# Optimization experiments

Measured on AMD Instinct MI355X. Metric: run time of the kernel, lower is better.

The kernel has to match this reference:

```python
import jax, jax.numpy as jnp
import numpy as np


def _apply_1q(state, U, wire):
    # state: (B,) + (2,)*n big-endian (wire 0 = axis 1, Pennylane convention)
    # U: (2,2) shared or (B,2,2) per-sample
    s = jnp.moveaxis(state, wire + 1, 1)
    eq = 'bij,bj...->bi...' if U.ndim == 3 else 'ij,bj...->bi...'
    s = jnp.einsum(eq, U, s)
    return jnp.moveaxis(s, 1, wire + 1)


def _rx(theta):  # theta: (B,) -> (B,2,2)
    c = jnp.cos(theta / 2).astype(jnp.complex64)
    s = (-1j * jnp.sin(theta / 2)).astype(jnp.complex64)
    return jnp.stack([jnp.stack([c, s], -1), jnp.stack([s, c], -1)], -2)


def _ry(theta):  # theta: (B,) -> (B,2,2)
    c = jnp.cos(theta / 2).astype(jnp.complex64)
    s = jnp.sin(theta / 2).astype(jnp.complex64)
    return jnp.stack([jnp.stack([c, -s], -1), jnp.stack([s, c], -1)], -2)


def _rot(phi, theta, omega):  # Pennylane Rot = RZ(omega) RY(theta) RZ(phi)
    c = jnp.cos(theta / 2)
    s = jnp.sin(theta / 2)
    r0 = jnp.stack([jnp.exp(-1j * (phi + omega) / 2) * c,
                    -jnp.exp(1j * (phi - omega) / 2) * s])
    r1 = jnp.stack([jnp.exp(-1j * (phi - omega) / 2) * s,
                    jnp.exp(1j * (phi + omega) / 2) * c])
    return jnp.stack([r0, r1]).astype(jnp.complex64)


def _cnot_adj(state, ctrl):
    # CNOT(control=ctrl, target=ctrl+1): flip target axis on control=1 slice
    a0 = jax.lax.index_in_dim(state, 0, ctrl + 1, keepdims=True)
    a1 = jax.lax.index_in_dim(state, 1, ctrl + 1, keepdims=True)
    return jnp.concatenate([a0, jnp.flip(a1, axis=ctrl + 2)], axis=ctrl + 1)


def _forward(state_batch, weights, head_w, head_b):
    L, n, _ = weights.shape
    B = state_batch.shape[0]
    psi = jnp.zeros((B, 2 ** n), jnp.complex64).at[:, 0].set(1.0)
    psi = psi.reshape((B,) + (2,) * n)
    # angle encoding (only first two features are used, as in the torch module)
    psi = _apply_1q(psi, _rx(state_batch[:, 0]), 0)
    psi = _apply_1q(psi, _ry(state_batch[:, 1]), 1)
    for l in range(L):
        for w in range(n):
            psi = _apply_1q(psi, _rot(weights[l, w, 0], weights[l, w, 1], weights[l, w, 2]), w)
        for i in range(n - 1):
            psi = _cnot_adj(psi, i)
    probs = psi.real ** 2 + psi.imag ** 2  # (B,) + (2,)*n
    feats = []
    for w in range(n):  # expval PauliZ on each wire
        p = probs.sum(axis=tuple(a for a in range(1, n + 1) if a != w + 1))
        feats.append(p[:, 0] - p[:, 1])
    features = jnp.stack(feats, axis=-1)  # (B, n)
    return (features @ head_w.T + head_b).squeeze(-1)  # (B,)


def setup_inputs() -> dict:
    key = jax.random.key(0)
    k1, k2, k3 = jax.random.split(key, 3)
    B, n, L = 8192, 12, 8
    return {
        'state_batch': jax.random.normal(k1, (B, 8), jnp.float32),
        'weights': jax.random.normal(k2, (L, n, 3), jnp.float32),
        'head_w': jax.random.normal(k3, (1, n), jnp.float32) / np.float32(np.sqrt(n)),
        'head_b': jnp.zeros((1,), jnp.float32),
    }


def reference(state_batch, weights, head_w, head_b):
    return _forward(state_batch, weights, head_w, head_b)
```

## Files before the change

kernel.cpp:

```cpp
#include <hip/hip_runtime.h>
#include <hip/hip_fp16.h>


typedef __half2 h2;
typedef _Float16 f16;
typedef __attribute__((ext_vector_type(8))) _Float16 f16x8;
typedef __attribute__((ext_vector_type(16))) float f32x16;

struct Gate32 { float a, b, c, d; };

#define SGN2 0x80008000
#define Z16 f32x16{0,0,0,0,0,0,0,0,0,0,0,0,0,0,0,0}

__device__ __forceinline__ float bpermf(int addr4, float v) {
    return __int_as_float(__builtin_amdgcn_ds_bpermute(addr4, __float_as_int(v)));
}
__device__ __forceinline__ int bci(h2 v)  { return __builtin_bit_cast(int, v); }
__device__ __forceinline__ h2 bch2(int v) { return __builtin_bit_cast(h2, v); }
__device__ __forceinline__ int g6(int x)  { return (x ^ (x >> 1)) & 63; }
__device__ __forceinline__ int moff(int row, int unit) {
    return row * 128 + ((unit ^ (row & 7)) << 4);
}
__device__ __forceinline__ f16x8 fneg8(f16x8 v) {
    int4 x = __builtin_bit_cast(int4, v);
    x.x ^= SGN2; x.y ^= SGN2; x.z ^= SGN2; x.w ^= SGN2;
    return __builtin_bit_cast(f16x8, x);
}
__device__ __forceinline__ f32x16 MFMA(f16x8 a, f16x8 b, f32x16 c) {
    return __builtin_amdgcn_mfma_f32_32x32x16_f16(a, b, c, 0, 0, 0);
}

struct C2 { float r, i; };
__device__ __forceinline__ C2 cmul(C2 x, C2 y) {
    return { x.r*y.r - x.i*y.i, x.r*y.i + x.i*y.r };
}
__device__ __forceinline__ C2 gent(const Gate32 g, int bi, int bj) {
    const float re = (bi == bj) ? g.a : (bi ? g.c : -g.c);
    const float im = (bi == bj) ? (bi ? g.b : -g.b) : -g.d;
    return { re, im };
}

__global__ void coeff_kernel(const float* __restrict__ wts, Gate32* __restrict__ tbl) {
    const int g = threadIdx.x;
    if (g >= 96) return;
    const int l = g / 12, w = g % 12;
    const float* lw = wts + l*36 + w*3;
    float ch, sh, ca, sa, cb, sb;
    __sincosf(0.5f*lw[1],           &sh, &ch);
    __sincosf(0.5f*(lw[0]+lw[2]),   &sa, &ca);
    __sincosf(0.5f*(lw[0]-lw[2]),   &sb, &cb);
    Gate32 r; r.a = ca*ch; r.b = sa*ch; r.c = cb*sh; r.d = sb*sh;
    tbl[g] = r;
}

__global__ __launch_bounds__(256, 1)
void sim_kernel(const Gate32* __restrict__ tbl, float2* __restrict__ cols) {
    extern __shared__ char smem[];
    char* Lr = smem;
    char* Li = smem + 8192;
    char* Rr = smem + 16384;
    char* Ri = smem + 24576;
    char* Sr = smem + 32768;
    char* Si = smem + 40960;
    char* Ur = smem + 49152;
    char* Ui = smem + 57344;
    float* KLr = (float*)(smem + 65536);
    float* KLi = KLr + 64;  float* KRr = KLr + 128; float* KRi = KLr + 192;
    f16* KLpr = (f16*)(KLr + 256);
    f16* KLpi = KLpr + 64;  f16* KRpr = KLpr + 128; f16* KRpi = KLpr + 192;

    const int tid  = threadIdx.x;
    const int lane = tid & 63;
    const int wid  = tid >> 6;
    const int b    = blockIdx.x;
    const int lo5  = lane & 31, hi = (lane >> 5) & 1;

    {
        const int4 z = make_int4(0, 0, 0, 0);
#pragma unroll
        for (int u = 0; u < 2; ++u) {
            const int idx = u * 256 + tid;
            const int row = idx >> 3, un = idx & 7;
            *(int4*)(Sr + moff(row, un)) = z;
            *(int4*)(Si + moff(row, un)) = z;
        }
    }
    __syncthreads();
    if (tid == 0) {
        const int row = 16 * b;
        *(f16*)(Sr + moff(row, 0)) = (f16)1.0f;
    }
    __syncthreads();

#pragma unroll 1
    for (int l = 0; l < 8; ++l) {
        const Gate32* gl = tbl + l * 12;
        if (tid < 64) {
            const int ip = tid >> 3, jp = tid & 7;
            const int i2 = (ip>>2)&1, i1 = (ip>>1)&1, i0 = ip&1;
            const int j2 = (jp>>2)&1, j1 = (jp>>1)&1, j0 = jp&1;
            const C2 kl  = cmul(cmul(gent(gl[0],i2,j2), gent(gl[1],i1,j1)), gent(gl[2],i0,j0));
            const C2 klp = cmul(cmul(gent(gl[3],i2,j2), gent(gl[4],i1,j1)), gent(gl[5],i0,j0));
            const C2 kr  = cmul(cmul(gent(gl[6],i2,j2), gent(gl[7],i1,j1)), gent(gl[8],i0,j0));
            const C2 krp = cmul(cmul(gent(gl[9],i2,j2), gent(gl[10],i1,j1)), gent(gl[11],i0,j0));
            KLr[tid] = kl.r;  KLi[tid] = kl.i;
            KRr[tid] = kr.r;  KRi[tid] = kr.i;
            KLpr[tid] = (f16)klp.r;  KLpi[tid] = (f16)klp.i;
            KRpr[tid] = (f16)krp.r;  KRpi[tid] = (f16)krp.i;
        }
        __syncthreads();
        {
            const int r = tid & 63, rh = r >> 3, rl = r & 7;
            const int side = (tid >> 6) & 1;
            const int hsel = tid >> 7;
            const float* xr4 = side ? (KRr + rh*8) : (KLr + rh*8);
            const float* xi4 = side ? (KRi + rh*8) : (KLi + rh*8);
            const int4 pyr = *(const int4*)((side ? KRpr : KLpr) + rl*8);
            const int4 pyi = *(const int4*)((side ? KRpi : KLpi) + rl*8);
            const h2 yr[4] = { bch2(pyr.x), bch2(pyr.y), bch2(pyr.z), bch2(pyr.w) };
            const h2 yi[4] = { bch2(pyi.x), bch2(pyi.y), bch2(pyi.z), bch2(pyi.w) };
            char* Pr = side ? Rr : Lr;
            char* Pi = side ? Ri : Li;
#pragma unroll
            for (int q = 0; q < 4; ++q) {
                const int hk = 4*hsel + q;
                const h2 xr2  = __float2half2_rn(xr4[hk]);
                const h2 xi2  = __float2half2_rn(xi4[hk]);
                const h2 nxi2 = bch2(bci(xi2) ^ SGN2);
                h2 oR[4], oI[4];
#pragma unroll
                for (int t = 0; t < 4; ++t) {
                    oR[t] = __hfma2(nxi2, yi[t], __hmul2(xr2, yr[t]));
                    oI[t] = __hfma2(xi2,  yr[t], __hmul2(xr2, yi[t]));
                }
                *(int4*)(Pr + moff(r, hk)) = make_int4(bci(oR[0]), bci(oR[1]), bci(oR[2]), bci(oR[3]));
                *(int4*)(Pi + moff(r, hk)) = make_int4(bci(oI[0]), bci(oI[1]), bci(oI[2]), bci(oI[3]));
            }
        }
        __syncthreads();
        {
            const int mt = wid >> 1, nt = wid & 1;
            f16x8 asr[4], asi[4], brr[4], bri[4];
            const int arow = 32*mt + lo5;
            const int brow = g6(32*nt + lo5);
#pragma unroll
            for (int kc = 0; kc < 4; ++kc) {
                const int un = 2*kc + hi;
                asr[kc] = *(const f16x8*)(Sr + moff(arow, un));
                asi[kc] = *(const f16x8*)(Si + moff(arow, un));
                brr[kc] = *(const f16x8*)(Rr + moff(brow, un));
                bri[kc] = *(const f16x8*)(Ri + moff(brow, un));
            }
            f32x16 ur = Z16, ui = Z16;
#pragma unroll
            for (int kc = 0; kc < 4; ++kc) {
                const f16x8 nri = fneg8(bri[kc]);
                ur = MFMA(asr[kc], brr[kc], ur);
                ur = MFMA(asi[kc], nri,     ur);
                ui = MFMA(asr[kc], bri[kc], ui);
                ui = MFMA(asi[kc], brr[kc], ui);
            }
            const int urow = 32*nt + lo5;
#pragma unroll
            for (int gg = 0; gg < 4; ++gg) {
                const h2 p0 = __floats2half2_rn(ur[4*gg+0], ur[4*gg+1]);
                const h2 p1 = __floats2half2_rn(ur[4*gg+2], ur[4*gg+3]);
                *(int2*)(Ur + moff(urow, 4*mt+gg) + 8*hi) = make_int2(bci(p0), bci(p1));
                const h2 q0 = __floats2half2_rn(ui[4*gg+0], ui[4*gg+1]);
                const h2 q1 = __floats2half2_rn(ui[4*gg+2], ui[4*gg+3]);
                *(int2*)(Ui + moff(urow, 4*mt+gg) + 8*hi) = make_int2(bci(q0), bci(q1));
            }
        }
        __syncthreads();
        {
            const int nt2 = wid >> 1, mt2 = wid & 1;
            f16x8 a1r[4], a1i[4], a2r[4], a2i[4];
            const int r1 = 32*nt2 + lo5, r2 = r1 ^ 63;
#pragma unroll
            for (int kc = 0; kc < 4; ++kc) {
                const int un = 2*kc + hi;
                a1r[kc] = *(const f16x8*)(Ur + moff(r1, un));
                a1i[kc] = *(const f16x8*)(Ui + moff(r1, un));
                a2r[kc] = *(const f16x8*)(Ur + moff(r2, un));
                a2i[kc] = *(const f16x8*)(Ui + moff(r2, un));
            }
            const int m = 32*mt2 + lo5;
            const int lrow = g6(m);
            f16x8 blr[4], bli[4];
#pragma unroll
            for (int kc = 0; kc < 4; ++kc) {
                const int un = 2*kc + hi;
                blr[kc] = *(const f16x8*)(Lr + moff(lrow, un));
                bli[kc] = *(const f16x8*)(Li + moff(lrow, un));
            }
            f32x16 w1r = Z16, w1i = Z16, w2r = Z16, w2i = Z16;
#pragma unroll
            for (int kc = 0; kc < 4; ++kc) {
                const f16x8 nbli = fneg8(bli[kc]);
                w1r = MFMA(a1r[kc], blr[kc], w1r);
                w1r = MFMA(a1i[kc], nbli,    w1r);
                w1i = MFMA(a1r[kc], bli[kc], w1i);
                w1i = MFMA(a1i[kc], blr[kc], w1i);
                w2r = MFMA(a2r[kc], blr[kc], w2r);
                w2r = MFMA(a2i[kc], nbli,    w2r);
                w2i = MFMA(a2r[kc], bli[kc], w2i);
                w2i = MFMA(a2i[kc], blr[kc], w2i);
            }
            const bool odd = (m & 1);
            if (l < 7) {
#pragma unroll
                for (int gg = 0; gg < 4; ++gg) {
                    float s0 = odd ? w2r[4*gg+0] : w1r[4*gg+0];
                    float s1 = odd ? w2r[4*gg+1] : w1r[4*gg+1];
                    float s2 = odd ? w2r[4*gg+2] : w1r[4*gg+2];
                    float s3 = odd ? w2r[4*gg+3] : w1r[4*gg+3];
                    *(int2*)(Sr + moff(m, 4*nt2+gg) + 8*hi) =
                        make_int2(bci(__floats2half2_rn(s0, s1)),
                                  bci(__floats2half2_rn(s2, s3)));
                    s0 = odd ? w2i[4*gg+0] : w1i[4*gg+0];
                    s1 = odd ? w2i[4*gg+1] : w1i[4*gg+1];
                    s2 = odd ? w2i[4*gg+2] : w1i[4*gg+2];
                    s3 = odd ? w2i[4*gg+3] : w1i[4*gg+3];
                    *(int2*)(Si + moff(m, 4*nt2+gg) + 8*hi) =
                        make_int2(bci(__floats2half2_rn(s0, s1)),
                                  bci(__floats2half2_rn(s2, s3)));
                }
            } else {
#pragma unroll
                for (int gg = 0; gg < 4; ++gg)
#pragma unroll
                for (int e = 0; e < 4; ++e) {
                    const int n = 32*nt2 + 8*gg + 4*hi + e;
                    const int r = 4*gg + e;
                    const float vr = odd ? w2r[r] : w1r[r];
                    const float vi = odd ? w2i[r] : w1i[r];
                    cols[b*4096 + (m << 6) + n] = make_float2(vr, vi);
                }
            }
        }
        __syncthreads();
    }
}

__global__ __launch_bounds__(256)
void finish_kernel(const float* __restrict__ sb,
                   const float2* __restrict__ cols,
                   const float* __restrict__ hw,
                   const float* __restrict__ hb,
                   float* __restrict__ out, int B) {
    const int tid  = threadIdx.x;
    const int lane = tid & 63, wid = tid >> 6;

    float hwv[12];
#pragma unroll
    for (int w = 0; w < 12; ++w) hwv[w] = hw[w];

    float Klo = 0.f;
#pragma unroll
    for (int w = 4; w < 12; ++w)
        Klo += ((tid >> (11 - w)) & 1) ? -hwv[w] : hwv[w];

    float g[10];
#pragma unroll
    for (int m = 0; m < 10; ++m) g[m] = 0.f;

#pragma unroll 1
    for (int it = 0; it < 16; ++it) {
        const int q = (it << 8) | tid;
        const float2 c0 = cols[q];
        const float2 c1 = cols[4096  + q];
        const float2 c2 = cols[8192  + q];
        const float2 c3 = cols[12288 + q];
        float K = Klo;
#pragma unroll
        for (int w = 0; w < 4; ++w)
            K += ((it >> (3 - w)) & 1) ? -hwv[w] : hwv[w];
        g[0] += K * (c0.x*c0.x + c0.y*c0.y);
        g[1] += K * (c1.x*c1.x + c1.y*c1.y);
        g[2] += K * (c2.x*c2.x + c2.y*c2.y);
        g[3] += K * (c3.x*c3.x + c3.y*c3.y);
        g[4] += K * (c0.x*c1.x + c0.y*c1.y);
        g[5] += K * (c2.x*c3.x + c2.y*c3.y);
        g[6] += K * (c0.x*c2.y - c0.y*c2.x);
        g[7] += K * (c0.x*c3.y - c0.y*c3.x);
        g[8] += K * (c1.x*c2.y - c1.y*c2.x);
        g[9] += K * (c1.x*c3.y - c1.y*c3.x);
    }

    __shared__ float gsh[4][10];
#pragma unroll
    for (int m = 0; m < 10; ++m) {
#pragma unroll
        for (int off = 1; off < 64; off <<= 1)
            g[m] += bpermf((lane ^ off) << 2, g[m]);
    }
    if (lane == 0) {
#pragma unroll
        for (int m = 0; m < 10; ++m) gsh[wid][m] = g[m];
    }
    __syncthreads();
    float G[10];
#pragma unroll
    for (int m = 0; m < 10; ++m) {
        const float s = gsh[0][m] + gsh[1][m] + gsh[2][m] + gsh[3][m];
        G[m] = (m < 4) ? s : 2.f * s;
    }

    const int i = blockIdx.x * 256 + tid;
    if (i < B) {
        const float2 x = *reinterpret_cast<const float2*>(sb + i*8);
        float c0, s0, c1, s1;
        __sincosf(0.5f * x.x, &s0, &c0);
        __sincosf(0.5f * x.y, &s1, &c1);
        const float a0 = c0*c1, a1 = c0*s1, a2 = s0*c1, a3 = s0*s1;
        const float r = G[0]*a0*a0 + G[1]*a1*a1 + G[2]*a2*a2 + G[3]*a3*a3
                      + G[4]*(a0*a1) + G[5]*(a2*a3)
                      + G[6]*(a0*a2) + G[7]*(a0*a3)
                      + G[8]*(a1*a2) + G[9]*(a1*a3);
        out[i] = r + hb[0];
    }
}

extern "C" void kernel_launch(void* const* d_in, const int* in_sizes, int n_in,
                              void* d_out, int out_size, void* d_ws, size_t ws_size,
                              hipStream_t stream) {
    const float* sb  = (const float*)d_in[0];
    const float* wts = (const float*)d_in[1];
    const float* hw  = (const float*)d_in[2];
    const float* hb  = (const float*)d_in[3];
    float* out = (float*)d_out;
    Gate32* tbl  = (Gate32*)d_ws;
    float2* cols = (float2*)((char*)d_ws + 4096);
    const int B = in_sizes[0] / 8;
    coeff_kernel <<<1, 128, 0, stream>>>(wts, tbl);
    sim_kernel   <<<4, 256, 67072, stream>>>(tbl, cols);
    finish_kernel<<<(B + 255)/256, 256, 0, stream>>>(sb, cols, hw, hb, out, B);
}
```

Baseline: 93.90 us.

## Fuse coefficient, simulation and finish kernels into one launch with flag sync

Merges the three kernel launches into a single grid. The first four blocks compute the gate table in shared memory and run the state simulation, then publish completion through a global atomic counter. The remaining blocks spin on that counter before doing the reduction and per-sample output. This removes two launch boundaries and the gate-table round trip through global memory. In exchange it adds a memset, relies on the simulation blocks being scheduled alongside the spinning ones (deadlock risk if they are not), and raises the shared-memory request for every block, including the finish blocks.

```diff
diff --git a/kernel.cpp b/kernel.cpp
--- a/kernel.cpp
+++ b/kernel.cpp
@@ -40,284 +40,295 @@
     return { re, im };
 }
 
-__global__ void coeff_kernel(const float* __restrict__ wts, Gate32* __restrict__ tbl) {
-    const int g = threadIdx.x;
-    if (g >= 96) return;
-    const int l = g / 12, w = g % 12;
-    const float* lw = wts + l*36 + w*3;
-    float ch, sh, ca, sa, cb, sb;
-    __sincosf(0.5f*lw[1],           &sh, &ch);
-    __sincosf(0.5f*(lw[0]+lw[2]),   &sa, &ca);
-    __sincosf(0.5f*(lw[0]-lw[2]),   &sb, &cb);
-    Gate32 r; r.a = ca*ch; r.b = sa*ch; r.c = cb*sh; r.d = sb*sh;
-    tbl[g] = r;
-}
-
 __global__ __launch_bounds__(256, 1)
-void sim_kernel(const Gate32* __restrict__ tbl, float2* __restrict__ cols) {
+void fused_kernel(const float* __restrict__ wts,
+                  const float* __restrict__ sb,
+                  const float* __restrict__ hw,
+                  const float* __restrict__ hb,
+                  float* __restrict__ out,
+                  int* __restrict__ flag,
+                  float2* __restrict__ cols, int B) {
     extern __shared__ char smem[];
-    char* Lr = smem;
-    char* Li = smem + 8192;
-    char* Rr = smem + 16384;
-    char* Ri = smem + 24576;
-    char* Sr = smem + 32768;
-    char* Si = smem + 40960;
-    char* Ur = smem + 49152;
-    char* Ui = smem + 57344;
-    float* KLr = (float*)(smem + 65536);
-    float* KLi = KLr + 64;  float* KRr = KLr + 128; float* KRi = KLr + 192;
-    f16* KLpr = (f16*)(KLr + 256);
-    f16* KLpi = KLpr + 64;  f16* KRpr = KLpr + 128; f16* KRpi = KLpr + 192;
-
-    const int tid  = threadIdx.x;
-    const int lane = tid & 63;
-    const int wid  = tid >> 6;
-    const int b    = blockIdx.x;
-    const int lo5  = lane & 31, hi = (lane >> 5) & 1;
-
-    {
-        const int4 z = make_int4(0, 0, 0, 0);
-#pragma unroll
-        for (int u = 0; u < 2; ++u) {
-            const int idx = u * 256 + tid;
-            const int row = idx >> 3, un = idx & 7;
-            *(int4*)(Sr + moff(row, un)) = z;
-            *(int4*)(Si + moff(row, un)) = z;
-        }
-    }
-    __syncthreads();
-    if (tid == 0) {
-        const int row = 16 * b;
-        *(f16*)(Sr + moff(row, 0)) = (f16)1.0f;
-    }
-    __syncthreads();
+    const int tid = threadIdx.x;
+
+    if (blockIdx.x < 4) {
+        char* Lr = smem;
+        char* Li = smem + 8192;
+        char* Rr = smem + 16384;
+        char* Ri = smem + 24576;
+        char* Sr = smem + 32768;
+        char* Si = smem + 40960;
+        char* Ur = smem + 49152;
+        char* Ui = smem + 57344;
+        float* KLr = (float*)(smem + 65536);
+        float* KLi = KLr + 64;  float* KRr = KLr + 128; float* KRi = KLr + 192;
+        f16* KLpr = (f16*)(smem + 66560);
+        f16* KLpi = KLpr + 64;  f16* KRpr = KLpr + 128; f16* KRpi = KLpr + 192;
+        Gate32* gt = (Gate32*)(smem + 67072);
+
+        const int lane = tid & 63;
+        const int wid  = tid >> 6;
+        const int b    = blockIdx.x;
+        const int lo5  = lane & 31, hi = (lane >> 5) & 1;
+
+        if (tid < 96) {
+            const int l = tid / 12, w = tid % 12;
+            const float* lw = wts + l*36 + w*3;
+            float ch, sh, ca, sa, cb, sb_;
+            __sincosf(0.5f*lw[1],         &sh, &ch);
+            __sincosf(0.5f*(lw[0]+lw[2]), &sa, &ca);
+            __sincosf(0.5f*(lw[0]-lw[2]), &sb_, &cb);
+            Gate32 r; r.a = ca*ch; r.b = sa*ch; r.c = cb*sh; r.d = sb_*sh;
+            gt[tid] = r;
+        }
+        {
+            const int4 z = make_int4(0, 0, 0, 0);
+#pragma unroll
+            for (int u = 0; u < 2; ++u) {
+                const int idx = u * 256 + tid;
+                const int row = idx >> 3, un = idx & 7;
+                *(int4*)(Sr + moff(row, un)) = z;
+                *(int4*)(Si + moff(row, un)) = z;
+            }
+        }
+        __syncthreads();
+        if (tid == 0) {
+            const int row = 16 * b;
+            *(f16*)(Sr + moff(row, 0)) = (f16)1.0f;
+        }
+        __syncthreads();
 
 #pragma unroll 1
-    for (int l = 0; l < 8; ++l) {
-        const Gate32* gl = tbl + l * 12;
-        if (tid < 64) {
-            const int ip = tid >> 3, jp = tid & 7;
-            const int i2 = (ip>>2)&1, i1 = (ip>>1)&1, i0 = ip&1;
-            const int j2 = (jp>>2)&1, j1 = (jp>>1)&1, j0 = jp&1;
-            const C2 kl  = cmul(cmul(gent(gl[0],i2,j2), gent(gl[1],i1,j1)), gent(gl[2],i0,j0));
-            const C2 klp = cmul(cmul(gent(gl[3],i2,j2), gent(gl[4],i1,j1)), gent(gl[5],i0,j0));
-            const C2 kr  = cmul(cmul(gent(gl[6],i2,j2), gent(gl[7],i1,j1)), gent(gl[8],i0,j0));
-            const C2 krp = cmul(cmul(gent(gl[9],i2,j2), gent(gl[10],i1,j1)), gent(gl[11],i0,j0));
-            KLr[tid] = kl.r;  KLi[tid] = kl.i;
-            KRr[tid] = kr.r;  KRi[tid] = kr.i;
-            KLpr[tid] = (f16)klp.r;  KLpi[tid] = (f16)klp.i;
-            KRpr[tid] = (f16)krp.r;  KRpi[tid] = (f16)krp.i;
-        }
-        __syncthreads();
-        {
-            const int r = tid & 63, rh = r >> 3, rl = r & 7;
-            const int side = (tid >> 6) & 1;
-            const int hsel = tid >> 7;
-            const float* xr4 = side ? (KRr + rh*8) : (KLr + rh*8);
-            const float* xi4 = side ? (KRi + rh*8) : (KLi + rh*8);
-            const int4 pyr = *(const int4*)((side ? KRpr : KLpr) + rl*8);
-            const int4 pyi = *(const int4*)((side ? KRpi : KLpi) + rl*8);
-            const h2 yr[4] = { bch2(pyr.x), bch2(pyr.y), bch2(pyr.z), bch2(pyr.w) };
-            const h2 yi[4] = { bch2(pyi.x), bch2(pyi.y), bch2(pyi.z), bch2(pyi.w) };
-            char* Pr = side ? Rr : Lr;
-            char* Pi = side ? Ri : Li;
-#pragma unroll
-            for (int q = 0; q < 4; ++q) {
-                const int hk = 4*hsel + q;
-                const h2 xr2  = __float2half2_rn(xr4[hk]);
-                const h2 xi2  = __float2half2_rn(xi4[hk]);
-                const h2 nxi2 = bch2(bci(xi2) ^ SGN2);
-                h2 oR[4], oI[4];
-#pragma unroll
-                for (int t = 0; t < 4; ++t) {
-                    oR[t] = __hfma2(nxi2, yi[t], __hmul2(xr2, yr[t]));
-                    oI[t] = __hfma2(xi2,  yr[t], __hmul2(xr2, yi[t]));
-                }
-                *(int4*)(Pr + moff(r, hk)) = make_int4(bci(oR[0]), bci(oR[1]), bci(oR[2]), bci(oR[3]));
-                *(int4*)(Pi + moff(r, hk)) = make_int4(bci(oI[0]), bci(oI[1]), bci(oI[2]), bci(oI[3]));
-            }
-        }
-        __syncthreads();
-        {
-            const int mt = wid >> 1, nt = wid & 1;
-            f16x8 asr[4], asi[4], brr[4], bri[4];
-            const int arow = 32*mt + lo5;
-            const int brow = g6(32*nt + lo5);
-#pragma unroll
-            for (int kc = 0; kc < 4; ++kc) {
-                const int un = 2*kc + hi;
-                asr[kc] = *(const f16x8*)(Sr + moff(arow, un));
-                asi[kc] = *(const f16x8*)(Si + moff(arow, un));
-                brr[kc] = *(const f16x8*)(Rr + moff(brow, un));
-                bri[kc] = *(const f16x8*)(Ri + moff(brow, un));
-            }
-            f32x16 ur = Z16, ui = Z16;
-#pragma unroll
-            for (int kc = 0; kc < 4; ++kc) {
-                const f16x8 nri = fneg8(bri[kc]);
-                ur = MFMA(asr[kc], brr[kc], ur);
-                ur = MFMA(asi[kc], nri,     ur);
-                ui = MFMA(asr[kc], bri[kc], ui);
-                ui = MFMA(asi[kc], brr[kc], ui);
-            }
-            const int urow = 32*nt + lo5;
-#pragma unroll
-            for (int gg = 0; gg < 4; ++gg) {
-                const h2 p0 = __floats2half2_rn(ur[4*gg+0], ur[4*gg+1]);
-                const h2 p1 = __floats2half2_rn(ur[4*gg+2], ur[4*gg+3]);
-                *(int2*)(Ur + moff(urow, 4*mt+gg) + 8*hi) = make_int2(bci(p0), bci(p1));
-                const h2 q0 = __floats2half2_rn(ui[4*gg+0], ui[4*gg+1]);
-                const h2 q1 = __floats2half2_rn(ui[4*gg+2], ui[4*gg+3]);
-                *(int2*)(Ui + moff(urow, 4*mt+gg) + 8*hi) = make_int2(bci(q0), bci(q1));
-            }
-        }
-        __syncthreads();
-        {
-            const int nt2 = wid >> 1, mt2 = wid & 1;
-            f16x8 a1r[4], a1i[4], a2r[4], a2i[4];
-            const int r1 = 32*nt2 + lo5, r2 = r1 ^ 63;
-#pragma unroll
-            for (int kc = 0; kc < 4; ++kc) {
-                const int un = 2*kc + hi;
-                a1r[kc] = *(const f16x8*)(Ur + moff(r1, un));
-                a1i[kc] = *(const f16x8*)(Ui + moff(r1, un));
-                a2r[kc] = *(const f16x8*)(Ur + moff(r2, un));
-                a2i[kc] = *(const f16x8*)(Ui + moff(r2, un));
-            }
-            const int m = 32*mt2 + lo5;
-            const int lrow = g6(m);
-            f16x8 blr[4], bli[4];
-#pragma unroll
-            for (int kc = 0; kc < 4; ++kc) {
-                const int un = 2*kc + hi;
-                blr[kc] = *(const f16x8*)(Lr + moff(lrow, un));
-                bli[kc] = *(const f16x8*)(Li + moff(lrow, un));
-            }
-            f32x16 w1r = Z16, w1i = Z16, w2r = Z16, w2i = Z16;
-#pragma unroll
-            for (int kc = 0; kc < 4; ++kc) {
-                const f16x8 nbli = fneg8(bli[kc]);
-                w1r = MFMA(a1r[kc], blr[kc], w1r);
-                w1r = MFMA(a1i[kc], nbli,    w1r);
-                w1i = MFMA(a1r[kc], bli[kc], w1i);
-                w1i = MFMA(a1i[kc], blr[kc], w1i);
-                w2r = MFMA(a2r[kc], blr[kc], w2r);
-                w2r = MFMA(a2i[kc], nbli,    w2r);
-                w2i = MFMA(a2r[kc], bli[kc], w2i);
-                w2i = MFMA(a2i[kc], blr[kc], w2i);
-            }
-            const bool odd = (m & 1);
-            if (l < 7) {
+        for (int l = 0; l < 8; ++l) {
+            const Gate32* gl = gt + l * 12;
+            if (tid < 64) {
+                const int ip = tid >> 3, jp = tid & 7;
+                const int i2 = (ip>>2)&1, i1 = (ip>>1)&1, i0 = ip&1;
+                const int j2 = (jp>>2)&1, j1 = (jp>>1)&1, j0 = jp&1;
+                const C2 kl  = cmul(cmul(gent(gl[0],i2,j2), gent(gl[1],i1,j1)), gent(gl[2],i0,j0));
+                const C2 klp = cmul(cmul(gent(gl[3],i2,j2), gent(gl[4],i1,j1)), gent(gl[5],i0,j0));
+                const C2 kr  = cmul(cmul(gent(gl[6],i2,j2), gent(gl[7],i1,j1)), gent(gl[8],i0,j0));
+                const C2 krp = cmul(cmul(gent(gl[9],i2,j2), gent(gl[10],i1,j1)), gent(gl[11],i0,j0));
+                KLr[tid] = kl.r;  KLi[tid] = kl.i;
+                KRr[tid] = kr.r;  KRi[tid] = kr.i;
+                KLpr[tid] = (f16)klp.r;  KLpi[tid] = (f16)klp.i;
+                KRpr[tid] = (f16)krp.r;  KRpi[tid] = (f16)krp.i;
+            }
+            __syncthreads();
+            {
+                const int r = tid & 63, rh = r >> 3, rl = r & 7;
+                const int side = (tid >> 6) & 1;
+                const int hsel = tid >> 7;
+                const float* xr4 = side ? (KRr + rh*8) : (KLr + rh*8);
+                const float* xi4 = side ? (KRi + rh*8) : (KLi + rh*8);
+                const int4 pyr = *(const int4*)((side ? KRpr : KLpr) + rl*8);
+                const int4 pyi = *(const int4*)((side ? KRpi : KLpi) + rl*8);
+                const h2 yr[4] = { bch2(pyr.x), bch2(pyr.y), bch2(pyr.z), bch2(pyr.w) };
+                const h2 yi[4] = { bch2(pyi.x), bch2(pyi.y), bch2(pyi.z), bch2(pyi.w) };
+                char* Pr = side ? Rr : Lr;
+                char* Pi = side ? Ri : Li;
+#pragma unroll
+                for (int q = 0; q < 4; ++q) {
+                    const int hk = 4*hsel + q;
+                    const h2 xr2  = __float2half2_rn(xr4[hk]);
+                    const h2 xi2  = __float2half2_rn(xi4[hk]);
+                    const h2 nxi2 = bch2(bci(xi2) ^ SGN2);
+                    h2 oR[4], oI[4];
+#pragma unroll
+                    for (int t = 0; t < 4; ++t) {
+                        oR[t] = __hfma2(nxi2, yi[t], __hmul2(xr2, yr[t]));
+                        oI[t] = __hfma2(xi2,  yr[t], __hmul2(xr2, yi[t]));
+                    }
+                    *(int4*)(Pr + moff(r, hk)) = make_int4(bci(oR[0]), bci(oR[1]), bci(oR[2]), bci(oR[3]));
+                    *(int4*)(Pi + moff(r, hk)) = make_int4(bci(oI[0]), bci(oI[1]), bci(oI[2]), bci(oI[3]));
+                }
+            }
+            __syncthreads();
+            {
+                const int mt = wid >> 1, nt = wid & 1;
+                f16x8 asr[4], asi[4], brr[4], bri[4];
+                const int arow = 32*mt + lo5;
+                const int brow = g6(32*nt + lo5);
+#pragma unroll
+                for (int kc = 0; kc < 4; ++kc) {
+                    const int un = 2*kc + hi;
+                    asr[kc] = *(const f16x8*)(Sr + moff(arow, un));
+                    asi[kc] = *(const f16x8*)(Si + moff(arow, un));
+                    brr[kc] = *(const f16x8*)(Rr + moff(brow, un));
+                    bri[kc] = *(const f16x8*)(Ri + moff(brow, un));
+                }
+                f32x16 ur = Z16, ui = Z16;
+#pragma unroll
+                for (int kc = 0; kc < 4; ++kc) {
+                    const f16x8 nri = fneg8(bri[kc]);
+                    ur = MFMA(asr[kc], brr[kc], ur);
+                    ur = MFMA(asi[kc], nri,     ur);
+                    ui = MFMA(asr[kc], bri[kc], ui);
+                    ui = MFMA(asi[kc], brr[kc], ui);
+                }
+                const int urow = 32*nt + lo5;
 #pragma unroll
                 for (int gg = 0; gg < 4; ++gg) {
-                    float s0 = odd ? w2r[4*gg+0] : w1r[4*gg+0];
-                    float s1 = odd ? w2r[4*gg+1] : w1r[4*gg+1];
-                    float s2 = odd ? w2r[4*gg+2] : w1r[4*gg+2];
-                    float s3 = odd ? w2r[4*gg+3] : w1r[4*gg+3];
-                    *(int2*)(Sr + moff(m, 4*nt2+gg) + 8*hi) =
-                        make_int2(bci(__floats2half2_rn(s0, s1)),
-                                  bci(__floats2half2_rn(s2, s3)));
-                    s0 = odd ? w2i[4*gg+0] : w1i[4*gg+0];
-                    s1 = odd ? w2i[4*gg+1] : w1i[4*gg+1];
-                    s2 = odd ? w2i[4*gg+2] : w1i[4*gg+2];
-                    s3 = odd ? w2i[4*gg+3] : w1i[4*gg+3];
-                    *(int2*)(Si + moff(m, 4*nt2+gg) + 8*hi) =
-                        make_int2(bci(__floats2half2_rn(s0, s1)),
-                                  bci(__floats2half2_rn(s2, s3)));
-                }
-            } else {
-#pragma unroll
-                for (int gg = 0; gg < 4; ++gg)
-#pragma unroll
-                for (int e = 0; e < 4; ++e) {
-                    const int n = 32*nt2 + 8*gg + 4*hi + e;
-                    const int r = 4*gg + e;
-                    const float vr = odd ? w2r[r] : w1r[r];
-                    const float vi = odd ? w2i[r] : w1i[r];
-                    cols[b*4096 + (m << 6) + n] = make_float2(vr, vi);
-                }
-            }
-        }
-        __syncthreads();
-    }
-}
-
-__global__ __launch_bounds__(256)
-void finish_kernel(const float* __restrict__ sb,
-                   const float2* __restrict__ cols,
-                   const float* __restrict__ hw,
-                   const float* __restrict__ hb,
-                   float* __restrict__ out, int B) {
-    const int tid  = threadIdx.x;
-    const int lane = tid & 63, wid = tid >> 6;
-
-    float hwv[12];
-#pragma unroll
-    for (int w = 0; w < 12; ++w) hwv[w] = hw[w];
-
-    float Klo = 0.f;
-#pragma unroll
-    for (int w = 4; w < 12; ++w)
-        Klo += ((tid >> (11 - w)) & 1) ? -hwv[w] : hwv[w];
-
-    float g[10];
-#pragma unroll
-    for (int m = 0; m < 10; ++m) g[m] = 0.f;
+                    const h2 p0 = __floats2half2_rn(ur[4*gg+0], ur[4*gg+1]);
+                    const h2 p1 = __floats2half2_rn(ur[4*gg+2], ur[4*gg+3]);
+                    *(int2*)(Ur + moff(urow, 4*mt+gg) + 8*hi) = make_int2(bci(p0), bci(p1));
+                    const h2 q0 = __floats2half2_rn(ui[4*gg+0], ui[4*gg+1]);
+                    const h2 q1 = __floats2half2_rn(ui[4*gg+2], ui[4*gg+3]);
+                    *(int2*)(Ui + moff(urow, 4*mt+gg) + 8*hi) = make_int2(bci(q0), bci(q1));
+                }
+            }
+            __syncthreads();
+            {
+                const int nt2 = wid >> 1, mt2 = wid & 1;
+                f16x8 a1r[4], a1i[4], a2r[4], a2i[4];
+                const int r1 = 32*nt2 + lo5, r2 = r1 ^ 63;
+#pragma unroll
+                for (int kc = 0; kc < 4; ++kc) {
+                    const int un = 2*kc + hi;
+                    a1r[kc] = *(const f16x8*)(Ur + moff(r1, un));
+                    a1i[kc] = *(const f16x8*)(Ui + moff(r1, un));
+                    a2r[kc] = *(const f16x8*)(Ur + moff(r2, un));
+                    a2i[kc] = *(const f16x8*)(Ui + moff(r2, un));
+                }
+                const int m = 32*mt2 + lo5;
+                const int lrow = g6(m);
+                f16x8 blr[4], bli[4];
+#pragma unroll
+                for (int kc = 0; kc < 4; ++kc) {
+                    const int un = 2*kc + hi;
+                    blr[kc] = *(const f16x8*)(Lr + moff(lrow, un));
+                    bli[kc] = *(const f16x8*)(Li + moff(lrow, un));
+                }
+                f32x16 w1r = Z16, w1i = Z16, w2r = Z16, w2i = Z16;
+#pragma unroll
+                for (int kc = 0; kc < 4; ++kc) {
+                    const f16x8 nbli = fneg8(bli[kc]);
+                    w1r = MFMA(a1r[kc], blr[kc], w1r);
+                    w1r = MFMA(a1i[kc], nbli,    w1r);
+                    w1i = MFMA(a1r[kc], bli[kc], w1i);
+                    w1i = MFMA(a1i[kc], blr[kc], w1i);
+                    w2r = MFMA(a2r[kc], blr[kc], w2r);
+                    w2r = MFMA(a2i[kc], nbli,    w2r);
+                    w2i = MFMA(a2r[kc], bli[kc], w2i);
+                    w2i = MFMA(a2i[kc], blr[kc], w2i);
+                }
+                const bool odd = (m & 1);
+                if (l < 7) {
+#pragma unroll
+                    for (int gg = 0; gg < 4; ++gg) {
+                        float s0 = odd ? w2r[4*gg+0] : w1r[4*gg+0];
+                        float s1 = odd ? w2r[4*gg+1] : w1r[4*gg+1];
+                        float s2 = odd ? w2r[4*gg+2] : w1r[4*gg+2];
+                        float s3 = odd ? w2r[4*gg+3] : w1r[4*gg+3];
+                        *(int2*)(Sr + moff(m, 4*nt2+gg) + 8*hi) =
+                            make_int2(bci(__floats2half2_rn(s0, s1)),
+                                      bci(__floats2half2_rn(s2, s3)));
+                        s0 = odd ? w2i[4*gg+0] : w1i[4*gg+0];
+                        s1 = odd ? w2i[4*gg+1] : w1i[4*gg+1];
+                        s2 = odd ? w2i[4*gg+2] : w1i[4*gg+2];
+                        s3 = odd ? w2i[4*gg+3] : w1i[4*gg+3];
+                        *(int2*)(Si + moff(m, 4*nt2+gg) + 8*hi) =
+                            make_int2(bci(__floats2half2_rn(s0, s1)),
+                                      bci(__floats2half2_rn(s2, s3)));
+                    }
+                } else {
+#pragma unroll
+                    for (int gg = 0; gg < 4; ++gg)
+#pragma unroll
+                    for (int e = 0; e < 4; ++e) {
+                        const int n = 32*nt2 + 8*gg + 4*hi + e;
+                        const int r = 4*gg + e;
+                        const float vr = odd ? w2r[r] : w1r[r];
+                        const float vi = odd ? w2i[r] : w1i[r];
+                        cols[b*4096 + (m << 6) + n] = make_float2(vr, vi);
+                    }
+                }
+            }
+            __syncthreads();
+        }
+        __threadfence();
+        __syncthreads();
+        if (tid == 0)
+            __hip_atomic_fetch_add(flag, 1, __ATOMIC_RELEASE, __HIP_MEMORY_SCOPE_AGENT);
+
+    } else {
+        float* gsh = (float*)smem;
+        const int lane = tid & 63, wid = tid >> 6;
+
+        float hwv[12];
+#pragma unroll
+        for (int w = 0; w < 12; ++w) hwv[w] = hw[w];
+
+        float Klo = 0.f;
+#pragma unroll
+        for (int w = 4; w < 12; ++w)
+            Klo += ((tid >> (11 - w)) & 1) ? -hwv[w] : hwv[w];
+
+        if (tid == 0) {
+            while (__hip_atomic_load(flag, __ATOMIC_ACQUIRE,
+                                     __HIP_MEMORY_SCOPE_AGENT) < 4) {}
+        }
+        __syncthreads();
+        __threadfence();
+
+        float g[10];
+#pragma unroll
+        for (int m = 0; m < 10; ++m) g[m] = 0.f;
 
 #pragma unroll 1
-    for (int it = 0; it < 16; ++it) {
-        const int q = (it << 8) | tid;
-        const float2 c0 = cols[q];
-        const float2 c1 = cols[4096  + q];
-        const float2 c2 = cols[8192  + q];
-        const float2 c3 = cols[12288 + q];
-        float K = Klo;
-#pragma unroll
-        for (int w = 0; w < 4; ++w)
-            K += ((it >> (3 - w)) & 1) ? -hwv[w] : hwv[w];
-        g[0] += K * (c0.x*c0.x + c0.y*c0.y);
-        g[1] += K * (c1.x*c1.x + c1.y*c1.y);
-        g[2] += K * (c2.x*c2.x + c2.y*c2.y);
-        g[3] += K * (c3.x*c3.x + c3.y*c3.y);
-        g[4] += K * (c0.x*c1.x + c0.y*c1.y);
-        g[5] += K * (c2.x*c3.x + c2.y*c3.y);
-        g[6] += K * (c0.x*c2.y - c0.y*c2.x);
-        g[7] += K * (c0.x*c3.y - c0.y*c3.x);
-        g[8] += K * (c1.x*c2.y - c1.y*c2.x);
-        g[9] += K * (c1.x*c3.y - c1.y*c3.x);
-    }
-
-    __shared__ float gsh[4][10];
-#pragma unroll
-    for (int m = 0; m < 10; ++m) {
-#pragma unroll
-        for (int off = 1; off < 64; off <<= 1)
-            g[m] += bpermf((lane ^ off) << 2, g[m]);
-    }
-    if (lane == 0) {
-#pragma unroll
-        for (int m = 0; m < 10; ++m) gsh[wid][m] = g[m];
-    }
-    __syncthreads();
-    float G[10];
-#pragma unroll
-    for (int m = 0; m < 10; ++m) {
-        const float s = gsh[0][m] + gsh[1][m] + gsh[2][m] + gsh[3][m];
-        G[m] = (m < 4) ? s : 2.f * s;
-    }
-
-    const int i = blockIdx.x * 256 + tid;
-    if (i < B) {
-        const float2 x = *reinterpret_cast<const float2*>(sb + i*8);
-        float c0, s0, c1, s1;
-        __sincosf(0.5f * x.x, &s0, &c0);
-        __sincosf(0.5f * x.y, &s1, &c1);
-        const float a0 = c0*c1, a1 = c0*s1, a2 = s0*c1, a3 = s0*s1;
-        const float r = G[0]*a0*a0 + G[1]*a1*a1 + G[2]*a2*a2 + G[3]*a3*a3
-                      + G[4]*(a0*a1) + G[5]*(a2*a3)
-                      + G[6]*(a0*a2) + G[7]*(a0*a3)
-                      + G[8]*(a1*a2) + G[9]*(a1*a3);
-        out[i] = r + hb[0];
+        for (int it = 0; it < 16; ++it) {
+            const int q = (it << 8) | tid;
+            const float2 c0 = cols[q];
+            const float2 c1 = cols[4096  + q];
+            const float2 c2 = cols[8192  + q];
+            const float2 c3 = cols[12288 + q];
+            float K = Klo;
+#pragma unroll
+            for (int w = 0; w < 4; ++w)
+                K += ((it >> (3 - w)) & 1) ? -hwv[w] : hwv[w];
+            g[0] += K * (c0.x*c0.x + c0.y*c0.y);
+            g[1] += K * (c1.x*c1.x + c1.y*c1.y);
+            g[2] += K * (c2.x*c2.x + c2.y*c2.y);
+            g[3] += K * (c3.x*c3.x + c3.y*c3.y);
+            g[4] += K * (c0.x*c1.x + c0.y*c1.y);
+            g[5] += K * (c2.x*c3.x + c2.y*c3.y);
+            g[6] += K * (c0.x*c2.y - c0.y*c2.x);
+            g[7] += K * (c0.x*c3.y - c0.y*c3.x);
+            g[8] += K * (c1.x*c2.y - c1.y*c2.x);
+            g[9] += K * (c1.x*c3.y - c1.y*c3.x);
+        }
+
+#pragma unroll
+        for (int m = 0; m < 10; ++m) {
+#pragma unroll
+            for (int off = 1; off < 64; off <<= 1)
+                g[m] += bpermf((lane ^ off) << 2, g[m]);
+        }
+        if (lane == 0) {
+#pragma unroll
+            for (int m = 0; m < 10; ++m) gsh[wid*10 + m] = g[m];
+        }
+        __syncthreads();
+        float G[10];
+#pragma unroll
+        for (int m = 0; m < 10; ++m) {
+            const float s = gsh[0*10+m] + gsh[1*10+m] + gsh[2*10+m] + gsh[3*10+m];
+            G[m] = (m < 4) ? s : 2.f * s;
+        }
+
+        const int i = (blockIdx.x - 4) * 256 + tid;
+        if (i < B) {
+            const float2 x = *reinterpret_cast<const float2*>(sb + i*8);
+            float c0, s0, c1, s1;
+            __sincosf(0.5f * x.x, &s0, &c0);
+            __sincosf(0.5f * x.y, &s1, &c1);
+            const float a0 = c0*c1, a1 = c0*s1, a2 = s0*c1, a3 = s0*s1;
+            const float r = G[0]*a0*a0 + G[1]*a1*a1 + G[2]*a2*a2 + G[3]*a3*a3
+                          + G[4]*(a0*a1) + G[5]*(a2*a3)
+                          + G[6]*(a0*a2) + G[7]*(a0*a3)
+                          + G[8]*(a1*a2) + G[9]*(a1*a3);
+            out[i] = r + hb[0];
+        }
     }
 }
 
@@ -329,10 +340,11 @@
     const float* hw  = (const float*)d_in[2];
     const float* hb  = (const float*)d_in[3];
     float* out = (float*)d_out;
-    Gate32* tbl  = (Gate32*)d_ws;
+    int*    flag = (int*)d_ws;
     float2* cols = (float2*)((char*)d_ws + 4096);
     const int B = in_sizes[0] / 8;
-    coeff_kernel <<<1, 128, 0, stream>>>(wts, tbl);
-    sim_kernel   <<<4, 256, 67072, stream>>>(tbl, cols);
-    finish_kernel<<<(B + 255)/256, 256, 0, stream>>>(sb, cols, hw, hb, out, B);
-}
+    hipMemsetAsync(d_ws, 0, 4, stream);
+    const int nfb = (B + 255) / 256;
+    fused_kernel<<<4 + nfb, 256, 68608, stream>>>(wts, sb, hw, hb, out,
+                                                  flag, cols, B);
+}
```

Result: no change. 95.30 us (+1.5%).

## Fuse gate-coefficient kernel into simulator and precompute next layer's matrices early

Applied to the files above, without the earlier changes.

The separate coefficient kernel is removed. Its sincos gate table is now computed inside sim_kernel into shared memory, which saves a kernel launch and a global round trip. The 8x8 kernel-matrix build for layer l+1 moves to the tail of iteration l, removing one block-wide barrier per layer. The first MFMA accumulation chain is also split into two independent accumulators to add instruction-level parallelism. The costs are slightly more LDS and some extra float adds, and the prologue relies on in-wave ordering between writing and reading the gate table.

```diff
diff --git a/kernel.cpp b/kernel.cpp
--- a/kernel.cpp
+++ b/kernel.cpp
@@ -40,21 +40,8 @@
     return { re, im };
 }
 
-__global__ void coeff_kernel(const float* __restrict__ wts, Gate32* __restrict__ tbl) {
-    const int g = threadIdx.x;
-    if (g >= 96) return;
-    const int l = g / 12, w = g % 12;
-    const float* lw = wts + l*36 + w*3;
-    float ch, sh, ca, sa, cb, sb;
-    __sincosf(0.5f*lw[1],           &sh, &ch);
-    __sincosf(0.5f*(lw[0]+lw[2]),   &sa, &ca);
-    __sincosf(0.5f*(lw[0]-lw[2]),   &sb, &cb);
-    Gate32 r; r.a = ca*ch; r.b = sa*ch; r.c = cb*sh; r.d = sb*sh;
-    tbl[g] = r;
-}
-
 __global__ __launch_bounds__(256, 1)
-void sim_kernel(const Gate32* __restrict__ tbl, float2* __restrict__ cols) {
+void sim_kernel(const float* __restrict__ wts, float2* __restrict__ cols) {
     extern __shared__ char smem[];
     char* Lr = smem;
     char* Li = smem + 8192;
@@ -66,8 +53,9 @@
     char* Ui = smem + 57344;
     float* KLr = (float*)(smem + 65536);
     float* KLi = KLr + 64;  float* KRr = KLr + 128; float* KRi = KLr + 192;
-    f16* KLpr = (f16*)(KLr + 256);
+    f16* KLpr = (f16*)(smem + 66560);
     f16* KLpi = KLpr + 64;  f16* KRpr = KLpr + 128; f16* KRpi = KLpr + 192;
+    Gate32* gt = (Gate32*)(smem + 67072);
 
     const int tid  = threadIdx.x;
     const int lane = tid & 63;
@@ -75,6 +63,16 @@
     const int b    = blockIdx.x;
     const int lo5  = lane & 31, hi = (lane >> 5) & 1;
 
+    if (tid < 96) {
+        const int l = tid / 12, w = tid % 12;
+        const float* lw = wts + l*36 + w*3;
+        float ch, sh, ca, sa, cb, sb_;
+        __sincosf(0.5f*lw[1],         &sh, &ch);
+        __sincosf(0.5f*(lw[0]+lw[2]), &sa, &ca);
+        __sincosf(0.5f*(lw[0]-lw[2]), &sb_, &cb);
+        Gate32 r; r.a = ca*ch; r.b = sa*ch; r.c = cb*sh; r.d = sb_*sh;
+        gt[tid] = r;
+    }
     {
         const int4 z = make_int4(0, 0, 0, 0);
 #pragma unroll
@@ -90,25 +88,24 @@
         const int row = 16 * b;
         *(f16*)(Sr + moff(row, 0)) = (f16)1.0f;
     }
+    if (tid < 64) {
+        const Gate32* gl = gt;
+        const int ip = tid >> 3, jp = tid & 7;
+        const int i2 = (ip>>2)&1, i1 = (ip>>1)&1, i0 = ip&1;
+        const int j2 = (jp>>2)&1, j1 = (jp>>1)&1, j0 = jp&1;
+        const C2 kl  = cmul(cmul(gent(gl[0],i2,j2), gent(gl[1],i1,j1)), gent(gl[2],i0,j0));
+        const C2 klp = cmul(cmul(gent(gl[3],i2,j2), gent(gl[4],i1,j1)), gent(gl[5],i0,j0));
+        const C2 kr  = cmul(cmul(gent(gl[6],i2,j2), gent(gl[7],i1,j1)), gent(gl[8],i0,j0));
+        const C2 krp = cmul(cmul(gent(gl[9],i2,j2), gent(gl[10],i1,j1)), gent(gl[11],i0,j0));
+        KLr[tid] = kl.r;  KLi[tid] = kl.i;
+        KRr[tid] = kr.r;  KRi[tid] = kr.i;
+        KLpr[tid] = (f16)klp.r;  KLpi[tid] = (f16)klp.i;
+        KRpr[tid] = (f16)krp.r;  KRpi[tid] = (f16)krp.i;
+    }
     __syncthreads();
 
 #pragma unroll 1
     for (int l = 0; l < 8; ++l) {
-        const Gate32* gl = tbl + l * 12;
-        if (tid < 64) {
-            const int ip = tid >> 3, jp = tid & 7;
-            const int i2 = (ip>>2)&1, i1 = (ip>>1)&1, i0 = ip&1;
-            const int j2 = (jp>>2)&1, j1 = (jp>>1)&1, j0 = jp&1;
-            const C2 kl  = cmul(cmul(gent(gl[0],i2,j2), gent(gl[1],i1,j1)), gent(gl[2],i0,j0));
-            const C2 klp = cmul(cmul(gent(gl[3],i2,j2), gent(gl[4],i1,j1)), gent(gl[5],i0,j0));
-            const C2 kr  = cmul(cmul(gent(gl[6],i2,j2), gent(gl[7],i1,j1)), gent(gl[8],i0,j0));
-            const C2 krp = cmul(cmul(gent(gl[9],i2,j2), gent(gl[10],i1,j1)), gent(gl[11],i0,j0));
-            KLr[tid] = kl.r;  KLi[tid] = kl.i;
-            KRr[tid] = kr.r;  KRi[tid] = kr.i;
-            KLpr[tid] = (f16)klp.r;  KLpi[tid] = (f16)klp.i;
-            KRpr[tid] = (f16)krp.r;  KRpi[tid] = (f16)krp.i;
-        }
-        __syncthreads();
         {
             const int r = tid & 63, rh = r >> 3, rl = r & 7;
             const int side = (tid >> 6) & 1;
@@ -151,23 +148,31 @@
                 brr[kc] = *(const f16x8*)(Rr + moff(brow, un));
                 bri[kc] = *(const f16x8*)(Ri + moff(brow, un));
             }
-            f32x16 ur = Z16, ui = Z16;
-#pragma unroll
-            for (int kc = 0; kc < 4; ++kc) {
+            f32x16 ur0 = Z16, ur1 = Z16, ui0 = Z16, ui1 = Z16;
+#pragma unroll
+            for (int kc = 0; kc < 2; ++kc) {
                 const f16x8 nri = fneg8(bri[kc]);
-                ur = MFMA(asr[kc], brr[kc], ur);
-                ur = MFMA(asi[kc], nri,     ur);
-                ui = MFMA(asr[kc], bri[kc], ui);
-                ui = MFMA(asi[kc], brr[kc], ui);
+                ur0 = MFMA(asr[kc], brr[kc], ur0);
+                ur0 = MFMA(asi[kc], nri,     ur0);
+                ui0 = MFMA(asr[kc], bri[kc], ui0);
+                ui0 = MFMA(asi[kc], brr[kc], ui0);
+            }
+#pragma unroll
+            for (int kc = 2; kc < 4; ++kc) {
+                const f16x8 nri = fneg8(bri[kc]);
+                ur1 = MFMA(asr[kc], brr[kc], ur1);
+                ur1 = MFMA(asi[kc], nri,     ur1);
+                ui1 = MFMA(asr[kc], bri[kc], ui1);
+                ui1 = MFMA(asi[kc], brr[kc], ui1);
             }
             const int urow = 32*nt + lo5;
 #pragma unroll
             for (int gg = 0; gg < 4; ++gg) {
-                const h2 p0 = __floats2half2_rn(ur[4*gg+0], ur[4*gg+1]);
-                const h2 p1 = __floats2half2_rn(ur[4*gg+2], ur[4*gg+3]);
+                const h2 p0 = __floats2half2_rn(ur0[4*gg+0]+ur1[4*gg+0], ur0[4*gg+1]+ur1[4*gg+1]);
+                const h2 p1 = __floats2half2_rn(ur0[4*gg+2]+ur1[4*gg+2], ur0[4*gg+3]+ur1[4*gg+3]);
                 *(int2*)(Ur + moff(urow, 4*mt+gg) + 8*hi) = make_int2(bci(p0), bci(p1));
-                const h2 q0 = __floats2half2_rn(ui[4*gg+0], ui[4*gg+1]);
-                const h2 q1 = __floats2half2_rn(ui[4*gg+2], ui[4*gg+3]);
+                const h2 q0 = __floats2half2_rn(ui0[4*gg+0]+ui1[4*gg+0], ui0[4*gg+1]+ui1[4*gg+1]);
+                const h2 q1 = __floats2half2_rn(ui0[4*gg+2]+ui1[4*gg+2], ui0[4*gg+3]+ui1[4*gg+3]);
                 *(int2*)(Ui + moff(urow, 4*mt+gg) + 8*hi) = make_int2(bci(q0), bci(q1));
             }
         }
@@ -237,6 +242,20 @@
                     cols[b*4096 + (m << 6) + n] = make_float2(vr, vi);
                 }
             }
+            if (l < 7 && tid < 64) {
+                const Gate32* gl2 = gt + (l+1) * 12;
+                const int ip = tid >> 3, jp = tid & 7;
+                const int i2 = (ip>>2)&1, i1 = (ip>>1)&1, i0 = ip&1;
+                const int j2 = (jp>>2)&1, j1 = (jp>>1)&1, j0 = jp&1;
+                const C2 kl  = cmul(cmul(gent(gl2[0],i2,j2), gent(gl2[1],i1,j1)), gent(gl2[2],i0,j0));
+                const C2 klp = cmul(cmul(gent(gl2[3],i2,j2), gent(gl2[4],i1,j1)), gent(gl2[5],i0,j0));
+                const C2 kr  = cmul(cmul(gent(gl2[6],i2,j2), gent(gl2[7],i1,j1)), gent(gl2[8],i0,j0));
+                const C2 krp = cmul(cmul(gent(gl2[9],i2,j2), gent(gl2[10],i1,j1)), gent(gl2[11],i0,j0));
+                KLr[tid] = kl.r;  KLi[tid] = kl.i;
+                KRr[tid] = kr.r;  KRi[tid] = kr.i;
+                KLpr[tid] = (f16)klp.r;  KLpi[tid] = (f16)klp.i;
+                KRpr[tid] = (f16)krp.r;  KRpi[tid] = (f16)krp.i;
+            }
         }
         __syncthreads();
     }
@@ -329,10 +348,8 @@
     const float* hw  = (const float*)d_in[2];
     const float* hb  = (const float*)d_in[3];
     float* out = (float*)d_out;
-    Gate32* tbl  = (Gate32*)d_ws;
     float2* cols = (float2*)((char*)d_ws + 4096);
     const int B = in_sizes[0] / 8;
-    coeff_kernel <<<1, 128, 0, stream>>>(wts, tbl);
-    sim_kernel   <<<4, 256, 67072, stream>>>(tbl, cols);
+    sim_kernel   <<<4, 256, 68608, stream>>>(wts, cols);
     finish_kernel<<<(B + 255)/256, 256, 0, stream>>>(sb, cols, hw, hb, out, B);
 }
```

Measured after the change: 89.41 us. 4.8% less time.
